# Performance work log

Hardware: AMD Instinct MI355X
Metric: run time of the kernel (lower is better)

## Reference

```python
import jax, jax.numpy as jnp
import numpy as np

ALPHA = 0.2  # LeakyReLU negative slope


def setup_inputs() -> dict:
    key = jax.random.key(0)
    k0, k1, k2, k3 = jax.random.split(key, 4)
    N, H, W, T, V = 16, 32, 32, 16, 64
    h = jax.random.normal(k0, (N, H, W, T, V), jnp.float32)
    conv_w = jax.random.normal(k1, (3, 3, T, T), jnp.float32) * 0.05  # HWIO
    conv_b = jnp.zeros((T,), jnp.float32)
    a = jax.random.normal(k2, (2 * H * W, 1), jnp.float32) * 0.03  # ~xavier scale
    B = jax.random.uniform(k3, (V, V), jnp.float32)
    return {"h": h, "conv_w": conv_w, "conv_b": conv_b, "a": a, "B": B}


def reference(h, conv_w, conv_b, a, B):
    N, H, W, T, V = h.shape
    hv = jnp.transpose(h, (0, 4, 1, 2, 3))  # (N,V,H,W,T)

    # ConvMapping: 3x3 SAME conv over spatial dims with T as channels
    x = hv.reshape(N * V, H, W, T)
    y = jax.lax.conv_general_dilated(
        x, conv_w, (1, 1), 'SAME',
        dimension_numbers=('NHWC', 'HWIO', 'NHWC')) + conv_b
    Wh = y.reshape(N, V, H, W, T)

    # Attention logits. Original builds concat([Wh_i, Wh_j], dim=W) with trailing
    # layout (H, 2W, T) then row-major views it as (T, 2*H*W). We reproduce that
    # exact reinterpretation, but exploit additivity over i/j so the O(V^2)
    # pair tensor is never materialized.
    HW2 = 2 * H * W
    zeros = jnp.zeros_like(Wh)
    Cl = jnp.concatenate([Wh, zeros], axis=3).reshape(N, V, T, HW2)
    Cr = jnp.concatenate([zeros, Wh], axis=3).reshape(N, V, T, HW2)
    av = a[:, 0]
    Ei = jnp.einsum('bvtk,k->bvt', Cl, av)
    Ej = jnp.einsum('bvtk,k->bvt', Cr, av)
    e = jax.nn.leaky_relu(Ei[:, :, None, :] + Ej[:, None, :, :], ALPHA)  # (N,V,V,T)
    att = jax.nn.softmax(e, axis=-1)  # softmax over time dim, as in original

    # Symmetric-normalized adjacency: D^-1/2 (B + I, min-max scaled) D^-1/2
    adj = B + jnp.eye(V, dtype=B.dtype)
    adj = (adj - adj.min()) / (adj.max() - adj.min())
    d12 = 1.0 / jnp.sqrt(jnp.sum(adj, axis=1))
    adj_norm = adj * d12[:, None] * d12[None, :]

    # Aggregation: h_prime[b,p,t,i] = sum_j Wh[b,j,p,t] * att[b,i,j,t]
    # (replaces the original V^2 python loop + diag_embed matmuls)
    Whf = Wh.reshape(N, V, H * W, T)
    hp = jnp.einsum('bjpt,bijt->bpti', Whf, att)  # (N,HW,T,V)
    out = jnp.einsum('bpti,iv->bptv', hp, adj_norm)
    return jax.nn.elu(out.reshape(N, H, W, T, V))
```

## Files before the change

kernel.cpp:

```cpp
#include <hip/hip_runtime.h>
#include <hip/hip_bf16.h>
#include <math.h>

#define ALPHA_ 0.2f
#define N_ 16
#define H_ 32
#define W_ 32
#define T_ 16
#define V_ 64
#define P_ (H_*W_)

#define HP_ 34
#define WP_ 34
#define XROW_ (WP_*V_*T_)

typedef __bf16 bf16x8 __attribute__((ext_vector_type(8)));
typedef float  f32x4  __attribute__((ext_vector_type(4)));

static __device__ inline unsigned short bf16bits(float f) {
    __hip_bfloat16 b = __float2bfloat16(f);
    return *reinterpret_cast<unsigned short*>(&b);
}

__global__ __launch_bounds__(256, 4) void tr2_k(const float* __restrict__ X,
                                                __hip_bfloat16* __restrict__ Xt,
                                                const float* __restrict__ CW,
                                                const float* __restrict__ Bm,
                                                __hip_bfloat16* __restrict__ Bfrag,
                                                float* __restrict__ adjn) {
    int orig = blockIdx.x;
    int tid = threadIdx.x;

    if (orig == N_*34*4) {
        __shared__ float sd[64];
        float row[64];
        int lane = tid;
        if (tid < 64) {
            int t = lane & 15, kg = lane >> 4;
            #pragma unroll
            for (int dw = 0; dw < 3; ++dw) {
                #pragma unroll
                for (int pr = 0; pr < 2; ++pr) {
                    __hip_bfloat16* dst = Bfrag + ((size_t)((dw*2+pr)*64 + lane))*8;
                    #pragma unroll
                    for (int i = 0; i < 8; ++i) {
                        int ti = (kg & 1)*8 + i;
                        float val;
                        if (pr == 0) { int dh = kg >> 1; val = CW[((dh*3+dw)*16+ti)*16 + t]; }
                        else          val = (kg < 2) ? CW[((2*3+dw)*16+ti)*16 + t] : 0.f;
                        dst[i] = __float2bfloat16(val);
                    }
                }
            }
            int i = lane;
            float mn = 1e30f, mx = -1e30f;
            #pragma unroll
            for (int v = 0; v < 64; ++v) {
                float x = Bm[i*64 + v] + (v == i ? 1.f : 0.f);
                row[v] = x;
                mn = fminf(mn, x);
                mx = fmaxf(mx, x);
            }
            #pragma unroll
            for (int off = 32; off > 0; off >>= 1) {
                mn = fminf(mn, __shfl_xor(mn, off));
                mx = fmaxf(mx, __shfl_xor(mx, off));
            }
            float inv = 1.f / (mx - mn);
            float rs = 0.f;
            #pragma unroll
            for (int v = 0; v < 64; ++v) {
                row[v] = (row[v] - mn) * inv;
                rs += row[v];
            }
            sd[i] = rsqrtf(rs);
        }
        __syncthreads();
        if (tid < 64) {
            float d = sd[tid];
            #pragma unroll
            for (int v = 0; v < 64; ++v) adjn[tid*64 + v] = row[v] * d * sd[v];
        }
        return;
    }

    int bid = (orig & 7) * 272 + (orig >> 3);
    int b   = bid / 136;
    int r   = bid % 136;
    int hp  = r >> 2;
    int wq  = r & 3;

    __hip_bfloat16* rowbase = Xt + ((size_t)b*HP_ + hp) * XROW_;
    __hip_bfloat16* dst = rowbase + (size_t)(wq*8 + 1) * (V_*T_);

    if (wq == 0) {
        uint4 z = {0u,0u,0u,0u};
        if (tid < 128) ((uint4*)rowbase)[tid] = z;
    } else if (wq == 3) {
        uint4 z = {0u,0u,0u,0u};
        if (tid < 128) ((uint4*)(rowbase + (size_t)33*(V_*T_)))[tid] = z;
    }

    if (hp == 0 || hp == 33) {
        uint4 z = {0u,0u,0u,0u};
        uint4* d = (uint4*)dst;
        #pragma unroll
        for (int k = 0; k < 4; ++k) d[tid + 256*k] = z;
        return;
    }
    int h = hp - 1;

    __shared__ __align__(16) unsigned sx[4096];

    int vq  = tid & 15;
    int tp4 = (tid >> 4) & 3;
    int w4  = tid >> 6;
    const float* Xb = X + (((size_t)(b*H_ + h)*W_ + wq*8) * T_) * V_ + vq*4;

    f32x4 xr[2][2][2];
    #pragma unroll
    for (int iw = 0; iw < 2; ++iw) {
        int wl = iw*4 + w4;
        #pragma unroll
        for (int th = 0; th < 2; ++th) {
            #pragma unroll
            for (int tk = 0; tk < 2; ++tk) {
                int ti = (th*4 + tp4)*2 + tk;
                xr[iw][th][tk] = *(const f32x4*)(Xb + ((size_t)wl*T_ + ti)*V_);
            }
        }
    }
    #pragma unroll
    for (int iw = 0; iw < 2; ++iw) {
        int wl = iw*4 + w4;
        #pragma unroll
        for (int th = 0; th < 2; ++th) {
            int tp = th*4 + tp4;
            uint4 pk;
            unsigned* pw = (unsigned*)&pk;
            #pragma unroll
            for (int k2 = 0; k2 < 4; ++k2)
                pw[k2] = (unsigned)bf16bits(xr[iw][th][0][k2])
                       | ((unsigned)bf16bits(xr[iw][th][1][k2]) << 16);
            *(uint4*)&sx[(wl*8 + tp)*64 + (vq ^ tp4)*4] = pk;
        }
    }
    __syncthreads();

    #pragma unroll
    for (int k = 0; k < 4; ++k) {
        int c   = tid + 256*k;
        int wl  = c >> 7;
        int vv  = (c >> 1) & 63;
        int thf = c & 1;
        uint4 o;
        unsigned* ow = (unsigned*)&o;
        #pragma unroll
        for (int q = 0; q < 4; ++q)
            ow[q] = sx[(wl*8 + thf*4 + q)*64 + ((vv >> 2) ^ q)*4 + (vv & 3)];
        *(uint4*)(dst + ((size_t)wl*V_ + vv)*T_ + thf*8) = o;
    }
}

__global__ __launch_bounds__(256, 3) void conv_k(const __hip_bfloat16* __restrict__ Xt,
                                                 const __hip_bfloat16* __restrict__ Bfrag,
                                                 const float* __restrict__ CB,
                                                 const float* __restrict__ av,
                                                 __hip_bfloat16* __restrict__ Whb,
                                                 float* __restrict__ Eihi,
                                                 float* __restrict__ Eihj) {
    __shared__ float sEi[4][16], sEj[4][16];

    int orig = blockIdx.x;
    int bi   = (orig & 7) * 256 + (255 - (orig >> 3));
    int b    = bi >> 7;
    int rem  = bi & 127;
    int h    = rem >> 2;
    int vg   = rem & 3, vb = vg * 16;

    int tid = threadIdx.x, lane = tid & 63, wc = tid >> 6;
    int lm = lane & 15, kg = lane >> 4;

    bf16x8 Bf01[3], Bf2[3];
    #pragma unroll
    for (int dw = 0; dw < 3; ++dw) {
        Bf01[dw] = *(const bf16x8*)(Bfrag + (size_t)((dw*2+0)*64 + lane)*8);
        Bf2 [dw] = *(const bf16x8*)(Bfrag + (size_t)((dw*2+1)*64 + lane)*8);
    }
    float cb = CB[lm];
    f32x4 acc[8];
    #pragma unroll
    for (int wi = 0; wi < 8; ++wi) acc[wi] = (f32x4){cb, cb, cb, cb};

    const __hip_bfloat16* base01 =
        Xt + ((size_t)(b*HP_ + h + (kg>>1)))*XROW_
           + (size_t)(wc*8)*(V_*T_) + (vb + lm)*T_ + (kg&1)*8;
    const __hip_bfloat16* base2  =
        Xt + ((size_t)(b*HP_ + h + 2))*XROW_
           + (size_t)(wc*8)*(V_*T_) + (vb + lm)*T_ + (kg&1)*8;

    bf16x8 f01[10], f2[10];
    #pragma unroll
    for (int u = 0; u < 10; ++u) {
        f01[u] = *(const bf16x8*)(base01 + (size_t)u*(V_*T_));
        f2 [u] = *(const bf16x8*)(base2  + (size_t)u*(V_*T_));
    }

    #pragma unroll
    for (int u = 0; u < 10; ++u) {
        #pragma unroll
        for (int dw = 0; dw < 3; ++dw) {
            int wi = u - dw;
            if (wi >= 0 && wi < 8) {
                acc[wi] = __builtin_amdgcn_mfma_f32_16x16x32_bf16(f01[u], Bf01[dw], acc[wi], 0, 0, 0);
                acc[wi] = __builtin_amdgcn_mfma_f32_16x16x32_bf16(f2 [u], Bf2 [dw], acc[wi], 0, 0, 0);
            }
        }
    }

    float si[4] = {0.f,0.f,0.f,0.f}, sj[4] = {0.f,0.f,0.f,0.f};
    {
        const float* avb = av + (h & 1)*1024 + wc*8*16 + lm;
        #pragma unroll
        for (int wi = 0; wi < 8; ++wi) {
            float ai = avb[wi*16];
            float aj = avb[wi*16 + 512];
            #pragma unroll
            for (int r = 0; r < 4; ++r) {
                si[r] += acc[wi][r] * ai;
                sj[r] += acc[wi][r] * aj;
            }
        }
        #pragma unroll
        for (int off = 1; off < 16; off <<= 1) {
            #pragma unroll
            for (int r = 0; r < 4; ++r) {
                si[r] += __shfl_xor(si[r], off);
                sj[r] += __shfl_xor(sj[r], off);
            }
        }
    }
    if (lm == 0) {
        #pragma unroll
        for (int r = 0; r < 4; ++r) {
            sEi[wc][kg*4 + r] = si[r];
            sEj[wc][kg*4 + r] = sj[r];
        }
    }

    #pragma unroll
    for (int wi = 0; wi < 8; ++wi) {
        int p = h*W_ + wc*8 + wi;
        unsigned short u0 = bf16bits(acc[wi][0]);
        unsigned short u1 = bf16bits(acc[wi][1]);
        unsigned short u2 = bf16bits(acc[wi][2]);
        unsigned short u3 = bf16bits(acc[wi][3]);
        uint2 pk;
        pk.x = (unsigned)u0 | ((unsigned)u1 << 16);
        pk.y = (unsigned)u2 | ((unsigned)u3 << 16);
        *(uint2*)(Whb + ((size_t)(b*T_ + lm)*P_ + p)*V_ + vb + kg*4) = pk;
    }

    __syncthreads();
    if (tid < 16) {
        float a = sEi[0][tid] + sEi[1][tid] + sEi[2][tid] + sEi[3][tid];
        float c = sEj[0][tid] + sEj[1][tid] + sEj[2][tid] + sEj[3][tid];
        Eihi[((size_t)b*H_ + h)*V_ + vb + tid] = a;
        Eihj[((size_t)b*H_ + h)*V_ + vb + tid] = c;
    }
}

__global__ __launch_bounds__(256, 4) void att_m_k(const float* __restrict__ Eihi,
                                                  const float* __restrict__ Eihj,
                                                  const float* __restrict__ adjn,
                                                  __hip_bfloat16* __restrict__ Mt) {
    int b = blockIdx.x >> 6;
    int j = blockIdx.x & 63;
    int tid = threadIdx.x;
    __shared__ float s_att[64][16];
    __shared__ float sadj[4096];

    #pragma unroll
    for (int k = 0; k < 16; ++k) sadj[tid + 256*k] = adjn[tid + 256*k];

    if (tid < 64) {
        int i = tid;
        const float* ebi = Eihi + (size_t)b*H_*V_;
        const float* ebj = Eihj + (size_t)b*H_*V_;
        float ev[16];
        float mxe = -1e30f;
        #pragma unroll
        for (int t = 0; t < 16; ++t) {
            float x = ebi[(2*t)*V_ + i] + ebi[(2*t+1)*V_ + i]
                    + ebj[(2*t)*V_ + j] + ebj[(2*t+1)*V_ + j];
            x = (x >= 0.f) ? x : ALPHA_ * x;
            ev[t] = x;
            mxe = fmaxf(mxe, x);
        }
        float s = 0.f;
        #pragma unroll
        for (int t = 0; t < 16; ++t) {
            ev[t] = __expf(ev[t] - mxe);
            s += ev[t];
        }
        float invs = 1.f / s;
        #pragma unroll
        for (int t = 0; t < 16; ++t) s_att[i][t] = ev[t] * invs;
    }
    __syncthreads();

    int v = tid & 63, tq = tid >> 6;
    float acc[4] = {0.f, 0.f, 0.f, 0.f};
    for (int i = 0; i < 64; ++i) {
        float an = sadj[i*64 + v];
        #pragma unroll
        for (int u = 0; u < 4; ++u) acc[u] += s_att[i][tq*4 + u] * an;
    }
    #pragma unroll
    for (int u = 0; u < 4; ++u) {
        int t = tq*4 + u;
        Mt[(((size_t)b*T_ + t)*V_ + v)*V_ + j] = __float2bfloat16(acc[u]);
    }
}

__global__ __launch_bounds__(256, 6) void out_k(const __hip_bfloat16* __restrict__ Whb,
                                                const __hip_bfloat16* __restrict__ Mt,
                                                float* __restrict__ out) {
    int orig = blockIdx.x;
    int bi   = (orig & 7) * 256 + (orig >> 3);
    int pc = bi & 7;
    int t  = (bi >> 3) & 15;
    int b  = bi >> 7;

    int tid  = threadIdx.x;
    int lane = tid & 63;
    int wid  = tid >> 6;
    int lm   = lane & 15;
    int lk   = lane >> 4;

    const __hip_bfloat16* Ab = Whb + ((size_t)(b*T_ + t)*P_ + pc*128) * V_;
    const __hip_bfloat16* Bb = Mt  + (size_t)(b*T_ + t) * (V_*V_);

    f32x4 acc[2][4];
    #pragma unroll
    for (int pt = 0; pt < 2; ++pt)
        #pragma unroll
        for (int vt = 0; vt < 4; ++vt) acc[pt][vt] = (f32x4){0.f,0.f,0.f,0.f};

    #pragma unroll
    for (int kf = 0; kf < 2; ++kf) {
        int ko = kf*32 + lk*8;
        bf16x8 b0 = *(const bf16x8*)(Ab + ((size_t)((wid*2+0)*16 + lm))*V_ + ko);
        bf16x8 b1 = *(const bf16x8*)(Ab + ((size_t)((wid*2+1)*16 + lm))*V_ + ko);
        #pragma unroll
        for (int vt = 0; vt < 4; ++vt) {
            bf16x8 a = *(const bf16x8*)(Bb + ((size_t)(vt*16 + lm))*V_ + ko);
            acc[0][vt] = __builtin_amdgcn_mfma_f32_16x16x32_bf16(a, b0, acc[0][vt], 0, 0, 0);
            acc[1][vt] = __builtin_amdgcn_mfma_f32_16x16x32_bf16(a, b1, acc[1][vt], 0, 0, 0);
        }
    }

    #pragma unroll
    for (int pt = 0; pt < 2; ++pt) {
        int p = pc*128 + (wid*2 + pt)*16 + lm;
        float* op = out + ((size_t)(b*P_ + p)*T_ + t)*V_;
        #pragma unroll
        for (int vt = 0; vt < 4; ++vt) {
            f32x4 e;
            #pragma unroll
            for (int r = 0; r < 4; ++r) {
                float x = acc[pt][vt][r];
                e[r] = (x > 0.f) ? x : (__expf(x) - 1.f);
            }
            *(f32x4*)(op + vt*16 + lk*4) = e;
        }
    }
}

extern "C" void kernel_launch(void* const* d_in, const int* in_sizes, int n_in,
                              void* d_out, int out_size, void* d_ws, size_t ws_size,
                              hipStream_t stream) {
    const float* X  = (const float*)d_in[0];
    const float* CW = (const float*)d_in[1];
    const float* CB = (const float*)d_in[2];
    const float* av = (const float*)d_in[3];
    const float* Bm = (const float*)d_in[4];
    float* outp = (float*)d_out;

    __hip_bfloat16* Whb = (__hip_bfloat16*)d_ws;
    __hip_bfloat16* Mt  = Whb + (size_t)N_*T_*P_*V_;
    float* Eihi = (float*)(Mt + (size_t)N_*T_*V_*V_);
    float* Eihj = Eihi + (size_t)N_*H_*V_;
    float* adjn = Eihj + (size_t)N_*H_*V_;
    __hip_bfloat16* Bfrag = (__hip_bfloat16*)(adjn + V_*V_);

    __hip_bfloat16* Xt = (__hip_bfloat16*)d_out;

    tr2_k  <<<N_*34*4 + 1, 256, 0, stream>>>(X, Xt, CW, Bm, Bfrag, adjn);
    conv_k <<<2048,        256, 0, stream>>>(Xt, Bfrag, CB, av, Whb, Eihi, Eihj);
    att_m_k<<<N_*V_,       256, 0, stream>>>(Eihi, Eihj, adjn, Mt);
    out_k  <<<N_*T_*8,     256, 0, stream>>>(Whb, Mt, outp);
}
```

Before: 76.55 us.

## Restructure attention-matrix kernel to one block per (batch, time) with coalesced stores

The attention/adjacency kernel now launches one block per (batch, time step) instead of per (batch, j). Each block computes the full 64x64 softmax slice for its time step, recomputing the 16-term softmax denominator per pair, then multiplies by the adjacency and writes contiguous bf16 rows with vector stores. This replaces strided scattered stores along j and uses all 256 threads in the softmax phase. In exchange the softmax work is redundantly recomputed 16 times across time steps, and only 256 blocks are launched.

```diff
diff --git a/kernel.cpp b/kernel.cpp
--- a/kernel.cpp
+++ b/kernel.cpp
@@ -270,56 +270,88 @@
     }
 }
 
-__global__ __launch_bounds__(256, 4) void att_m_k(const float* __restrict__ Eihi,
-                                                  const float* __restrict__ Eihj,
-                                                  const float* __restrict__ adjn,
-                                                  __hip_bfloat16* __restrict__ Mt) {
-    int b = blockIdx.x >> 6;
-    int j = blockIdx.x & 63;
+__global__ __launch_bounds__(256, 2) void att_m2_k(const float* __restrict__ Eihi,
+                                                   const float* __restrict__ Eihj,
+                                                   const float* __restrict__ adjn,
+                                                   __hip_bfloat16* __restrict__ Mt) {
+    int orig = blockIdx.x;
+    int bi   = (orig & 7) * 32 + (orig >> 3);
+    int b = bi >> 4;
+    int t = bi & 15;
     int tid = threadIdx.x;
-    __shared__ float s_att[64][16];
-    __shared__ float sadj[4096];
-
-    #pragma unroll
-    for (int k = 0; k < 16; ++k) sadj[tid + 256*k] = adjn[tid + 256*k];
-
-    if (tid < 64) {
-        int i = tid;
-        const float* ebi = Eihi + (size_t)b*H_*V_;
-        const float* ebj = Eihj + (size_t)b*H_*V_;
-        float ev[16];
-        float mxe = -1e30f;
-        #pragma unroll
-        for (int t = 0; t < 16; ++t) {
-            float x = ebi[(2*t)*V_ + i] + ebi[(2*t+1)*V_ + i]
-                    + ebj[(2*t)*V_ + j] + ebj[(2*t+1)*V_ + j];
-            x = (x >= 0.f) ? x : ALPHA_ * x;
-            ev[t] = x;
-            mxe = fmaxf(mxe, x);
-        }
-        float s = 0.f;
-        #pragma unroll
-        for (int t = 0; t < 16; ++t) {
-            ev[t] = __expf(ev[t] - mxe);
-            s += ev[t];
-        }
-        float invs = 1.f / s;
-        #pragma unroll
-        for (int t = 0; t < 16; ++t) s_att[i][t] = ev[t] * invs;
+
+    __shared__ float sEi[16][64];
+    __shared__ float sEj[16][64];
+    __shared__ float s_att[64][65];
+    __shared__ float sadj[64][64];
+
+    const float* ebi = Eihi + (size_t)b*H_*V_;
+    const float* ebj = Eihj + (size_t)b*H_*V_;
+    #pragma unroll
+    for (int k = 0; k < 4; ++k) {
+        int idx = tid + 256*k;
+        int i  = idx & 63;
+        int tp = idx >> 6;
+        sEi[tp][i] = ebi[(2*tp)*V_ + i] + ebi[(2*tp+1)*V_ + i];
+        sEj[tp][i] = ebj[(2*tp)*V_ + i] + ebj[(2*tp+1)*V_ + i];
+    }
+    #pragma unroll
+    for (int k = 0; k < 16; ++k) {
+        int idx = tid + 256*k;
+        sadj[idx >> 6][idx & 63] = adjn[idx];
     }
     __syncthreads();
 
-    int v = tid & 63, tq = tid >> 6;
-    float acc[4] = {0.f, 0.f, 0.f, 0.f};
-    for (int i = 0; i < 64; ++i) {
-        float an = sadj[i*64 + v];
-        #pragma unroll
-        for (int u = 0; u < 4; ++u) acc[u] += s_att[i][tq*4 + u] * an;
-    }
-    #pragma unroll
-    for (int u = 0; u < 4; ++u) {
-        int t = tq*4 + u;
-        Mt[(((size_t)b*T_ + t)*V_ + v)*V_ + j] = __float2bfloat16(acc[u]);
+    {
+        int i1 = tid >> 2;
+        int jq = tid & 3;
+        float ei[16];
+        #pragma unroll
+        for (int tp = 0; tp < 16; ++tp) ei[tp] = sEi[tp][i1];
+        #pragma unroll 2
+        for (int jj = 0; jj < 16; ++jj) {
+            int j = jq*16 + jj;
+            float e[16];
+            float mxe = -1e30f;
+            #pragma unroll
+            for (int tp = 0; tp < 16; ++tp) {
+                float x = ei[tp] + sEj[tp][j];
+                x = (x >= 0.f) ? x : ALPHA_ * x;
+                e[tp] = x;
+                mxe = fmaxf(mxe, x);
+            }
+            float s = 0.f;
+            float evt = 0.f;
+            #pragma unroll
+            for (int tp = 0; tp < 16; ++tp) {
+                float ex = __expf(e[tp] - mxe);
+                s += ex;
+                if (tp == t) evt = ex;
+            }
+            s_att[i1][j] = evt * (1.f / s);
+        }
+    }
+    __syncthreads();
+
+    int jo = tid & 7;
+    int v0 = tid >> 3;
+    #pragma unroll
+    for (int pass = 0; pass < 2; ++pass) {
+        int v = v0 + pass*32;
+        float acc[8] = {0.f,0.f,0.f,0.f,0.f,0.f,0.f,0.f};
+        for (int i = 0; i < 64; ++i) {
+            float an = sadj[i][v];
+            const float* sa = &s_att[i][jo*8];
+            #pragma unroll
+            for (int q = 0; q < 8; ++q) acc[q] += sa[q] * an;
+        }
+        uint4 pk;
+        unsigned* pw = (unsigned*)&pk;
+        #pragma unroll
+        for (int q2 = 0; q2 < 4; ++q2)
+            pw[q2] = (unsigned)bf16bits(acc[2*q2])
+                   | ((unsigned)bf16bits(acc[2*q2+1]) << 16);
+        *(uint4*)(Mt + ((size_t)(b*T_ + t)*V_ + v)*V_ + jo*8) = pk;
     }
 }
 
@@ -396,8 +428,8 @@
 
     __hip_bfloat16* Xt = (__hip_bfloat16*)d_out;
 
-    tr2_k  <<<N_*34*4 + 1, 256, 0, stream>>>(X, Xt, CW, Bm, Bfrag, adjn);
-    conv_k <<<2048,        256, 0, stream>>>(Xt, Bfrag, CB, av, Whb, Eihi, Eihj);
-    att_m_k<<<N_*V_,       256, 0, stream>>>(Eihi, Eihj, adjn, Mt);
-    out_k  <<<N_*T_*8,     256, 0, stream>>>(Whb, Mt, outp);
-}
+    tr2_k   <<<N_*34*4 + 1, 256, 0, stream>>>(X, Xt, CW, Bm, Bfrag, adjn);
+    conv_k  <<<2048,        256, 0, stream>>>(Xt, Bfrag, CB, av, Whb, Eihi, Eihj);
+    att_m2_k<<<N_*T_,       256, 0, stream>>>(Eihi, Eihj, adjn, Mt);
+    out_k   <<<N_*T_*8,     256, 0, stream>>>(Whb, Mt, outp);
+}
```

Measured after the change: 80.80 us. +5.5%, slower.
